# Kernel optimization log

Measured on AMD Instinct MI355X. Metric: run time of the kernel, lower is better.

The kernel has to match this reference:

```python
import jax, jax.numpy as jnp
import numpy as np

N = 25000
E = 400000
HIDDEN = 512
NH = 8
DH = HIDDEN // NH


def setup_inputs() -> dict:
    key = jax.random.key(0)
    ks = jax.random.split(key, 10)
    s = 1.0 / np.sqrt(HIDDEN)
    return {
        "h": jax.random.normal(ks[0], (N, HIDDEN), dtype=jnp.float32),
        "Wq": jax.random.normal(ks[1], (HIDDEN, HIDDEN), dtype=jnp.float32) * s,
        "bq": jnp.zeros((HIDDEN,), dtype=jnp.float32),
        "Wk": jax.random.normal(ks[2], (HIDDEN, HIDDEN), dtype=jnp.float32) * s,
        "bk": jnp.zeros((HIDDEN,), dtype=jnp.float32),
        "Wo": jax.random.normal(ks[3], (HIDDEN, HIDDEN), dtype=jnp.float32) * s,
        "bo": jnp.zeros((HIDDEN,), dtype=jnp.float32),
        "rows": jax.random.randint(ks[4], (E,), 0, N, dtype=jnp.int32),
        "cols": jax.random.randint(ks[5], (E,), 0, N, dtype=jnp.int32),
    }


def reference(h, Wq, bq, Wk, bk, Wo, bo, rows, cols):
    # Projections; reshape (N, dh, nh) exactly as the source does.
    q = (h @ Wq + bq).reshape(N, DH, NH)
    k = (h @ Wk + bk).reshape(N, DH, NH)
    v = k  # source bug kept faithfully: v = linear_k(h)

    # SDDMM: per-edge, per-head dot product (no 1/sqrt(dh) scaling in source).
    scores = jnp.einsum("edh,edh->eh", q[rows], k[cols])  # [E, NH]

    # Row-wise (source-node) segment softmax per head.
    m = jax.ops.segment_max(scores, rows, num_segments=N)       # [N, NH]
    ex = jnp.exp(scores - m[rows])                              # [E, NH]
    denom = jax.ops.segment_sum(ex, rows, num_segments=N)      # [N, NH]
    attn = ex / denom[rows]                                     # [E, NH]

    # SpMM: out[i] = sum_{j in nbr(i)} attn[ij] * v[j]
    msgs = attn[:, None, :] * v[cols]                           # [E, DH, NH]
    out = jax.ops.segment_sum(msgs, rows, num_segments=N)      # [N, DH, NH]

    return out.reshape(N, HIDDEN) @ Wo + bo
```

## Files before the change

kernel.cpp:

```cpp
#include <hip/hip_runtime.h>
#include <math.h>

typedef unsigned short u16;
typedef unsigned int u32;
typedef __attribute__((ext_vector_type(8))) _Float16 half8;
typedef __attribute__((ext_vector_type(8))) u16 ushort8;
typedef __attribute__((ext_vector_type(4))) float f32x4;

__device__ __forceinline__ float h2f(u16 u) {
    union { u16 u; _Float16 h; } c; c.u = u; return (float)c.h;
}
__device__ __forceinline__ u16 f2h(float f) {
    union { u16 u; _Float16 h; } c; c.h = (_Float16)f; return c.u;
}

__device__ __forceinline__ void gload16(void* lds, const void* g) {
    __builtin_amdgcn_global_load_lds(
        (const __attribute__((address_space(1))) u32*)g,
        (__attribute__((address_space(3))) u32*)lds,
        16, 0, 0);
}

template <int OUTMODE>
__global__ __launch_bounds__(256) void gemm_f16(
    const u16* __restrict__ A, const u16* __restrict__ Bt,
    const float* __restrict__ bias, void* __restrict__ Cout, int Mout)
{
    __shared__ __align__(16) u16 As0[4096], As1[4096], Bs0[4096], Bs1[4096];

    const int tid  = threadIdx.x;
    const int wave = tid >> 6;
    const int lane = tid & 63;
    const int m0 = blockIdx.x * 128;
    const int n0 = blockIdx.y * 128;
    const int wr = (wave >> 1) * 64;
    const int wc = (wave & 1) * 64;

    f32x4 acc[4][4];
#pragma unroll
    for (int i = 0; i < 4; ++i)
#pragma unroll
        for (int j = 0; j < 4; ++j) acc[i][j] = (f32x4){0.f, 0.f, 0.f, 0.f};

    const int srow  = lane >> 2;
    const int scolG = ((lane & 3) ^ ((srow >> 1) & 3)) * 8;
    const size_t gOffA = (size_t)(m0 + wave * 32 + srow) * 512 + scolG;
    const size_t gOffB = (size_t)(n0 + wave * 32 + srow) * 512 + scolG;
    const int lOff = wave * 1024 + srow * 32 + (lane & 3) * 8;

    const int fR = ((lane & 15) >> 1) & 3;
    const int paOff = (wr + (lane & 15)) * 32 + ((lane >> 4) ^ fR) * 8;
    const int pbOff = (wc + (lane & 15)) * 32 + ((lane >> 4) ^ fR) * 8;

    auto STAGE = [&](u16* sa, u16* sb, int ko) {
        gload16(sa + lOff,       A  + gOffA + ko);
        gload16(sa + lOff + 512, A  + gOffA + ko + 16 * 512);
        gload16(sb + lOff,       Bt + gOffB + ko);
        gload16(sb + lOff + 512, Bt + gOffB + ko + 16 * 512);
    };
    auto COMPUTE = [&](const u16* sa, const u16* sb) {
        half8 af[4], bf[4];
#pragma unroll
        for (int i = 0; i < 4; ++i) af[i] = *(const half8*)(sa + paOff + i * 512);
#pragma unroll
        for (int j = 0; j < 4; ++j) bf[j] = *(const half8*)(sb + pbOff + j * 512);
#pragma unroll
        for (int i = 0; i < 4; ++i)
#pragma unroll
            for (int j = 0; j < 4; ++j)
                acc[i][j] = __builtin_amdgcn_mfma_f32_16x16x32_f16(
                    af[i], bf[j], acc[i][j], 0, 0, 0);
    };

    STAGE(As0, Bs0, 0);
    __syncthreads();
#pragma unroll
    for (int kt = 0; kt < 16; kt += 2) {
        STAGE(As1, Bs1, (kt + 1) * 32);
        COMPUTE(As0, Bs0);
        __syncthreads();
        if (kt + 2 < 16) STAGE(As0, Bs0, (kt + 2) * 32);
        COMPUTE(As1, Bs1);
        __syncthreads();
    }

    const int ccol  = n0 + wc + (lane & 15);
    const int crow0 = m0 + wr + (lane >> 4) * 4;
#pragma unroll
    for (int j = 0; j < 4; ++j) {
        const float b = bias[ccol + j * 16];
#pragma unroll
        for (int i = 0; i < 4; ++i) {
#pragma unroll
            for (int r = 0; r < 4; ++r) {
                int row = crow0 + i * 16 + r;
                if (row < Mout) {
                    float v = acc[i][j][r] + b;
                    size_t off = (size_t)row * 512 + ccol + j * 16;
                    if (OUTMODE == 0) ((float*)Cout)[off] = v;
                    else              ((u16*)Cout)[off] = f2h(v);
                }
            }
        }
    }
}

__global__ __launch_bounds__(256) void conv_h(
    const float* __restrict__ h, u16* __restrict__ hh, int nN)
{
    int t = blockIdx.x * 256 + threadIdx.x;
    size_t e = (size_t)t * 8;
    int row = (int)(e >> 9);
    ushort8 o;
    if (row < nN) {
        f32x4 a = *(const f32x4*)(h + e);
        f32x4 b = *(const f32x4*)(h + e + 4);
        float x[8] = {a.x, a.y, a.z, a.w, b.x, b.y, b.z, b.w};
#pragma unroll
        for (int i = 0; i < 8; ++i) o[i] = f2h(x[i]);
    } else {
        o = (ushort8){0,0,0,0,0,0,0,0};
    }
    *(ushort8*)(hh + e) = o;
}

__global__ __launch_bounds__(256) void conv_w(
    const float* __restrict__ Wq, const float* __restrict__ Wk,
    const float* __restrict__ Wo, const float* __restrict__ bq,
    const float* __restrict__ bk,
    u16* __restrict__ Wqt, u16* __restrict__ Wkt, u16* __restrict__ Wot,
    float* __restrict__ bqp, float* __restrict__ bkp)
{
    __shared__ float T[64][65];
    const int tid = threadIdx.x;
    const int z = blockIdx.z;
    const int X = blockIdx.x * 64;
    const int Y = blockIdx.y * 64;

    const int r4 = tid >> 4;
    const int c4 = (tid & 15) * 4;
    if (z < 2) {
        const float* W = z ? Wk : Wq;
#pragma unroll
        for (int rr = 0; rr < 64; rr += 16) {
            f32x4 v = *(const f32x4*)(W + (size_t)(X + rr + r4) * 512 + Y + c4);
            T[rr + r4][c4 + 0] = v.x; T[rr + r4][c4 + 1] = v.y;
            T[rr + r4][c4 + 2] = v.z; T[rr + r4][c4 + 3] = v.w;
        }
    } else {
#pragma unroll
        for (int rr = 0; rr < 64; rr += 16) {
            int p2 = (rr + r4) * 8 + (X >> 6);
            f32x4 v = *(const f32x4*)(Wo + (size_t)p2 * 512 + Y + c4);
            T[rr + r4][c4 + 0] = v.x; T[rr + r4][c4 + 1] = v.y;
            T[rr + r4][c4 + 2] = v.z; T[rr + r4][c4 + 3] = v.w;
        }
    }
    __syncthreads();

    const int cc = tid >> 2;
    const int ks = (tid & 3) * 16;
    const int pc = Y + cc;
    const int ro = (z < 2) ? ((pc & 7) * 64 + (pc >> 3)) : pc;
    ushort8 h0, h1;
#pragma unroll
    for (int t = 0; t < 8; ++t) {
        h0[t] = f2h(T[ks + t][cc]);
        h1[t] = f2h(T[ks + 8 + t][cc]);
    }
    size_t o = (size_t)ro * 512 + X + ks;
    if (z == 0) {
        *(ushort8*)(Wqt + o) = h0; *(ushort8*)(Wqt + o + 8) = h1;
    } else if (z == 1) {
        *(ushort8*)(Wkt + o) = h0; *(ushort8*)(Wkt + o + 8) = h1;
    } else {
        *(ushort8*)(Wot + o) = h0; *(ushort8*)(Wot + o + 8) = h1;
        if (blockIdx.x == 0 && blockIdx.y == 0) {
            for (int b = tid; b < 512; b += 256) {
                int pp = (b & 63) * 8 + (b >> 6);
                bqp[b] = bq[pp];
                bkp[b] = bk[pp];
            }
        }
    }
}

__global__ void hist_kernel(const int* __restrict__ rows, int* __restrict__ deg, int E)
{
    int i = blockIdx.x * 256 + threadIdx.x;
    if (i < E) atomicAdd(&deg[rows[i]], 1);
}

#define SCAN_CHUNK 2048

__global__ __launch_bounds__(256) void scan_partial(
    const int* __restrict__ deg, int* __restrict__ bsum, int n)
{
    int base = blockIdx.x * SCAN_CHUNK;
    int t = threadIdx.x;
    int s = 0;
    for (int i = t; i < SCAN_CHUNK; i += 256) {
        int g = base + i;
        s += (g < n) ? deg[g] : 0;
    }
#pragma unroll
    for (int off = 1; off < 64; off <<= 1) s += __shfl_xor(s, off, 64);
    __shared__ int ws[4];
    if ((t & 63) == 0) ws[t >> 6] = s;
    __syncthreads();
    if (t == 0) bsum[blockIdx.x] = ws[0] + ws[1] + ws[2] + ws[3];
}

__global__ __launch_bounds__(64) void scan_bsum(
    int* __restrict__ bsum, int nb, int* __restrict__ rowptr, int n)
{
    int l = threadIdx.x;
    int v = (l < nb) ? bsum[l] : 0;
    int orig = v;
#pragma unroll
    for (int off = 1; off < 64; off <<= 1) {
        int x = __shfl_up(v, off, 64);
        if (l >= off) v += x;
    }
    if (l < nb) bsum[l] = v - orig;
    if (l == nb - 1) rowptr[n] = v;
}

__global__ __launch_bounds__(256) void scan_final(
    const int* __restrict__ deg, const int* __restrict__ bsum,
    int* __restrict__ rowptr, int* __restrict__ cursor, int n)
{
    int t = threadIdx.x;
    int base = blockIdx.x * SCAN_CHUNK + t * 8;
    int v[8];
    int s = 0;
#pragma unroll
    for (int i = 0; i < 8; ++i) {
        int g = base + i;
        v[i] = (g < n) ? deg[g] : 0;
        s += v[i];
    }
    int lane = t & 63, w = t >> 6;
    int inc = s;
#pragma unroll
    for (int off = 1; off < 64; off <<= 1) {
        int x = __shfl_up(inc, off, 64);
        if (lane >= off) inc += x;
    }
    __shared__ int wsum[4];
    if (lane == 63) wsum[w] = inc;
    __syncthreads();
    int excl = bsum[blockIdx.x] + inc - s;
    for (int i = 0; i < w; ++i) excl += wsum[i];
#pragma unroll
    for (int i = 0; i < 8; ++i) {
        int g = base + i;
        if (g < n) { rowptr[g] = excl; cursor[g] = excl; }
        excl += v[i];
    }
}

__global__ void scatter_kernel(const int* __restrict__ rows, const int* __restrict__ cols,
                               int* __restrict__ cursor, int* __restrict__ colc, int E)
{
    int i = blockIdx.x * 256 + threadIdx.x;
    if (i < E) {
        int pos = atomicAdd(&cursor[rows[i]], 1);
        colc[pos] = cols[i];
    }
}

__global__ __launch_bounds__(256) void node_agg(
    const u16* __restrict__ Qh, const u16* __restrict__ Kb,
    const int* __restrict__ rowptr, const int* __restrict__ colc,
    u16* __restrict__ aggb, int nN)
{
    int node = blockIdx.x * 4 + (threadIdx.x >> 6);
    int lane = threadIdx.x & 63;
    if (node >= nN) return;
    size_t base = (size_t)node * 512 + lane * 8;

    float q[8];
    {
        ushort8 qv = __builtin_nontemporal_load((const ushort8*)(Qh + base));
#pragma unroll
        for (int i = 0; i < 8; ++i) q[i] = h2f(qv[i]);
    }

    int start = rowptr[node];
    int deg   = rowptr[node + 1] - start;
    const int* cp = colc + start;
    const size_t loff = (size_t)lane * 8;

    float m = -__builtin_inff();
    float den = 0.f;
    float acc[8];
#pragma unroll
    for (int i = 0; i < 8; ++i) acc[i] = 0.f;

    if (deg > 0) {
        const int dl = deg - 1;
        ushort8 k0 = *(const ushort8*)(Kb + (size_t)cp[0] * 512 + loff);
        ushort8 k1 = *(const ushort8*)(Kb + (size_t)cp[1 < dl ? 1 : dl] * 512 + loff);
        ushort8 k2 = *(const ushort8*)(Kb + (size_t)cp[2 < dl ? 2 : dl] * 512 + loff);
        ushort8 k3 = *(const ushort8*)(Kb + (size_t)cp[3 < dl ? 3 : dl] * 512 + loff);
        for (int j = 0; j < deg; j += 4) {
            int i4 = j + 4 < dl ? j + 4 : dl;
            int i5 = j + 5 < dl ? j + 5 : dl;
            int i6 = j + 6 < dl ? j + 6 : dl;
            int i7 = j + 7 < dl ? j + 7 : dl;
            ushort8 n0 = *(const ushort8*)(Kb + (size_t)cp[i4] * 512 + loff);
            ushort8 n1 = *(const ushort8*)(Kb + (size_t)cp[i5] * 512 + loff);
            ushort8 n2 = *(const ushort8*)(Kb + (size_t)cp[i6] * 512 + loff);
            ushort8 n3 = *(const ushort8*)(Kb + (size_t)cp[i7] * 512 + loff);

            float kf0[8], kf1[8], kf2[8], kf3[8];
#pragma unroll
            for (int i = 0; i < 8; ++i) {
                kf0[i] = h2f(k0[i]); kf1[i] = h2f(k1[i]);
                kf2[i] = h2f(k2[i]); kf3[i] = h2f(k3[i]);
            }
            float p0 = 0.f, p1 = 0.f, p2 = 0.f, p3 = 0.f;
#pragma unroll
            for (int i = 0; i < 8; ++i) {
                p0 = fmaf(q[i], kf0[i], p0);
                p1 = fmaf(q[i], kf1[i], p1);
                p2 = fmaf(q[i], kf2[i], p2);
                p3 = fmaf(q[i], kf3[i], p3);
            }
#pragma unroll
            for (int off = 1; off < 8; off <<= 1) {
                p0 += __shfl_xor(p0, off, 64);
                p1 += __shfl_xor(p1, off, 64);
                p2 += __shfl_xor(p2, off, 64);
                p3 += __shfl_xor(p3, off, 64);
            }

            float pm = fmaxf(fmaxf(p0, p1), fmaxf(p2, p3));
            if (__any(pm > m + 8.f)) {
                float mn = fmaxf(m, pm);
                float sc = __expf(m - mn);
                den *= sc;
#pragma unroll
                for (int i = 0; i < 8; ++i) acc[i] *= sc;
                m = mn;
            }
            float w0 = __expf(p0 - m);
            float w1 = (j + 1 < deg) ? __expf(p1 - m) : 0.f;
            float w2 = (j + 2 < deg) ? __expf(p2 - m) : 0.f;
            float w3 = (j + 3 < deg) ? __expf(p3 - m) : 0.f;
            den += (w0 + w1) + (w2 + w3);
#pragma unroll
            for (int i = 0; i < 8; ++i)
                acc[i] = fmaf(w3, kf3[i], fmaf(w2, kf2[i],
                         fmaf(w1, kf1[i], fmaf(w0, kf0[i], acc[i]))));
            k0 = n0; k1 = n1; k2 = n2; k3 = n3;
        }
    }

    float inv = (deg > 0) ? 1.f / den : 0.f;
    ushort8 o;
#pragma unroll
    for (int i = 0; i < 8; ++i) o[i] = f2h(acc[i] * inv);
    __builtin_nontemporal_store(o, (ushort8*)(aggb + base));
}

extern "C" void kernel_launch(void* const* d_in, const int* in_sizes, int n_in,
                              void* d_out, int out_size, void* d_ws, size_t ws_size,
                              hipStream_t stream)
{
    const float* h  = (const float*)d_in[0];
    const float* Wq = (const float*)d_in[1];
    const float* bq = (const float*)d_in[2];
    const float* Wk = (const float*)d_in[3];
    const float* bk = (const float*)d_in[4];
    const float* Wo = (const float*)d_in[5];
    const float* bo = (const float*)d_in[6];
    const int* rows = (const int*)d_in[7];
    const int* cols = (const int*)d_in[8];
    float* out = (float*)d_out;

    const int HID = 512;
    const int nN  = in_sizes[0] / HID;
    const int E   = in_sizes[7];
    const int nPad = (nN + 127) & ~127;
    const int nb = (nN + SCAN_CHUNK - 1) / SCAN_CHUNK;

    char* w = (char*)d_ws;
    u16* Kb  = (u16*)w;  w += (size_t)nPad * HID * 2;
    u16* hh  = (u16*)w;  w += (size_t)nPad * HID * 2;
    u16* Qh  = (u16*)w;  w += (size_t)nPad * HID * 2;
    u16* Wqt = (u16*)w;  w += 512 * 512 * 2;
    u16* Wkt = (u16*)w;  w += 512 * 512 * 2;
    u16* Wot = (u16*)w;  w += 512 * 512 * 2;
    float* bqp = (float*)w;  w += 512 * 4;
    float* bkp = (float*)w;  w += 512 * 4;
    int* rowptr = (int*)w;   w += (size_t)(nN + 1) * 4;
    int* cursor = (int*)w;   w += (size_t)nN * 4;
    int* deg    = (int*)w;   w += (size_t)nN * 4;
    int* bsum   = (int*)w;   w += 64 * 4;
    int* colc   = (int*)w;

    hipMemsetAsync(deg, 0, (size_t)nN * sizeof(int), stream);
    hist_kernel<<<(E + 255) / 256, 256, 0, stream>>>(rows, deg, E);
    scan_partial<<<nb, 256, 0, stream>>>(deg, bsum, nN);
    scan_bsum<<<1, 64, 0, stream>>>(bsum, nb, rowptr, nN);
    scan_final<<<nb, 256, 0, stream>>>(deg, bsum, rowptr, cursor, nN);
    scatter_kernel<<<(E + 255) / 256, 256, 0, stream>>>(rows, cols, cursor, colc, E);

    conv_h<<<(nPad * (HID / 8) + 255) / 256, 256, 0, stream>>>(h, hh, nN);
    conv_w<<<dim3(8, 8, 3), 256, 0, stream>>>(Wq, Wk, Wo, bq, bk,
                                              Wqt, Wkt, Wot, bqp, bkp);

    dim3 gg(nPad / 128, 4);
    gemm_f16<1><<<gg, 256, 0, stream>>>(hh, Wqt, bqp, Qh, nPad);
    gemm_f16<1><<<gg, 256, 0, stream>>>(hh, Wkt, bkp, Kb, nPad);

    node_agg<<<(nN + 3) / 4, 256, 0, stream>>>(Qh, Kb, rowptr, colc, hh, nN);

    gemm_f16<0><<<gg, 256, 0, stream>>>(hh, Wot, bo, out, nN);
}
```

Before: 263.7 us.

## Fuse prep kernels, merge Q/K GEMMs, and use packed fp16 math in aggregation

Merges the h conversion, degree histogram and weight transpose into one prep launch. It folds the bsum scan into scan_final and runs the Q and K projections as one GEMM launch via blockIdx.z. The node aggregation now uses fdot2 for the dot products and packed fp16 accumulation for the weighted sum, with a tighter rescale threshold. The aim is fewer launches and less conversion ALU work. Accumulating in fp16 risks precision loss and overflow on high-degree nodes.

New measurement: 234.8 us. 1.12x faster.

```diff
diff --git a/kernel.cpp b/kernel.cpp
--- a/kernel.cpp
+++ b/kernel.cpp
@@ -4,15 +4,20 @@
 typedef unsigned short u16;
 typedef unsigned int u32;
 typedef __attribute__((ext_vector_type(8))) _Float16 half8;
+typedef __attribute__((ext_vector_type(2))) _Float16 half2v;
 typedef __attribute__((ext_vector_type(8))) u16 ushort8;
 typedef __attribute__((ext_vector_type(4))) float f32x4;
 
-__device__ __forceinline__ float h2f(u16 u) {
-    union { u16 u; _Float16 h; } c; c.u = u; return (float)c.h;
-}
 __device__ __forceinline__ u16 f2h(float f) {
     union { u16 u; _Float16 h; } c; c.h = (_Float16)f; return c.u;
 }
+
+#if __has_builtin(__builtin_amdgcn_fdot2)
+#define FDOT2(a, b, c) __builtin_amdgcn_fdot2((a), (b), (c), false)
+#else
+#define FDOT2(a, b, c) fmaf((float)(a)[0], (float)(b)[0], \
+                        fmaf((float)(a)[1], (float)(b)[1], (c)))
+#endif
 
 __device__ __forceinline__ void gload16(void* lds, const void* g) {
     __builtin_amdgcn_global_load_lds(
@@ -22,17 +27,13 @@
 }
 
 template <int OUTMODE>
-__global__ __launch_bounds__(256) void gemm_f16(
-    const u16* __restrict__ A, const u16* __restrict__ Bt,
-    const float* __restrict__ bias, void* __restrict__ Cout, int Mout)
-{
-    __shared__ __align__(16) u16 As0[4096], As1[4096], Bs0[4096], Bs1[4096];
-
+__device__ __forceinline__ void gemm_body(
+    const u16* A, const u16* Bt, const float* bias, void* Cout, int Mout,
+    int m0, int n0, u16* As0, u16* As1, u16* Bs0, u16* Bs1)
+{
     const int tid  = threadIdx.x;
     const int wave = tid >> 6;
     const int lane = tid & 63;
-    const int m0 = blockIdx.x * 128;
-    const int n0 = blockIdx.y * 128;
     const int wr = (wave >> 1) * 64;
     const int wc = (wave & 1) * 64;
 
@@ -105,37 +106,69 @@
     }
 }
 
-__global__ __launch_bounds__(256) void conv_h(
-    const float* __restrict__ h, u16* __restrict__ hh, int nN)
-{
-    int t = blockIdx.x * 256 + threadIdx.x;
-    size_t e = (size_t)t * 8;
-    int row = (int)(e >> 9);
-    ushort8 o;
-    if (row < nN) {
-        f32x4 a = *(const f32x4*)(h + e);
-        f32x4 b = *(const f32x4*)(h + e + 4);
-        float x[8] = {a.x, a.y, a.z, a.w, b.x, b.y, b.z, b.w};
-#pragma unroll
-        for (int i = 0; i < 8; ++i) o[i] = f2h(x[i]);
-    } else {
-        o = (ushort8){0,0,0,0,0,0,0,0};
-    }
-    *(ushort8*)(hh + e) = o;
-}
-
-__global__ __launch_bounds__(256) void conv_w(
+__global__ __launch_bounds__(256) void gemm_qk(
+    const u16* __restrict__ hh, const u16* __restrict__ Wqt,
+    const u16* __restrict__ Wkt, const float* __restrict__ bqp,
+    const float* __restrict__ bkp, u16* __restrict__ Qh,
+    u16* __restrict__ Kb, int nPad)
+{
+    __shared__ __align__(16) u16 As0[4096], As1[4096], Bs0[4096], Bs1[4096];
+    const u16* Bt = blockIdx.z ? Wkt : Wqt;
+    const float* bias = blockIdx.z ? bkp : bqp;
+    u16* out = blockIdx.z ? Kb : Qh;
+    gemm_body<1>(hh, Bt, bias, out, nPad, blockIdx.x * 128, blockIdx.y * 128,
+                 As0, As1, Bs0, Bs1);
+}
+
+__global__ __launch_bounds__(256) void gemm_wo(
+    const u16* __restrict__ A, const u16* __restrict__ Wot,
+    const float* __restrict__ bo, float* __restrict__ C, int Mout)
+{
+    __shared__ __align__(16) u16 As0[4096], As1[4096], Bs0[4096], Bs1[4096];
+    gemm_body<0>(A, Wot, bo, C, Mout, blockIdx.x * 128, blockIdx.y * 128,
+                 As0, As1, Bs0, Bs1);
+}
+
+__global__ __launch_bounds__(256) void prep(
+    const float* __restrict__ h, u16* __restrict__ hh, int nN,
+    const int* __restrict__ rows, int* __restrict__ deg, int E,
     const float* __restrict__ Wq, const float* __restrict__ Wk,
     const float* __restrict__ Wo, const float* __restrict__ bq,
     const float* __restrict__ bk,
     u16* __restrict__ Wqt, u16* __restrict__ Wkt, u16* __restrict__ Wot,
-    float* __restrict__ bqp, float* __restrict__ bkp)
+    float* __restrict__ bqp, float* __restrict__ bkp,
+    int nbH, int nbE)
 {
     __shared__ float T[64][65];
     const int tid = threadIdx.x;
-    const int z = blockIdx.z;
-    const int X = blockIdx.x * 64;
-    const int Y = blockIdx.y * 64;
+    const int b = blockIdx.x;
+
+    if (b < nbH) {
+        int t = b * 256 + tid;
+        size_t e = (size_t)t * 8;
+        int row = (int)(e >> 9);
+        ushort8 o;
+        if (row < nN) {
+            f32x4 a = *(const f32x4*)(h + e);
+            f32x4 bb = *(const f32x4*)(h + e + 4);
+            float x[8] = {a.x, a.y, a.z, a.w, bb.x, bb.y, bb.z, bb.w};
+#pragma unroll
+            for (int i = 0; i < 8; ++i) o[i] = f2h(x[i]);
+        } else {
+            o = (ushort8){0,0,0,0,0,0,0,0};
+        }
+        *(ushort8*)(hh + e) = o;
+        return;
+    }
+    if (b < nbH + nbE) {
+        int i = (b - nbH) * 256 + tid;
+        if (i < E) atomicAdd(&deg[rows[i]], 1);
+        return;
+    }
+    int rem = b - nbH - nbE;
+    const int z = rem >> 6;
+    const int X = (rem & 7) * 64;
+    const int Y = ((rem >> 3) & 7) * 64;
 
     const int r4 = tid >> 4;
     const int c4 = (tid & 15) * 4;
@@ -175,20 +208,14 @@
         *(ushort8*)(Wkt + o) = h0; *(ushort8*)(Wkt + o + 8) = h1;
     } else {
         *(ushort8*)(Wot + o) = h0; *(ushort8*)(Wot + o + 8) = h1;
-        if (blockIdx.x == 0 && blockIdx.y == 0) {
-            for (int b = tid; b < 512; b += 256) {
-                int pp = (b & 63) * 8 + (b >> 6);
-                bqp[b] = bq[pp];
-                bkp[b] = bk[pp];
-            }
-        }
-    }
-}
-
-__global__ void hist_kernel(const int* __restrict__ rows, int* __restrict__ deg, int E)
-{
-    int i = blockIdx.x * 256 + threadIdx.x;
-    if (i < E) atomicAdd(&deg[rows[i]], 1);
+        if (rem == 128) {
+            for (int bi = tid; bi < 512; bi += 256) {
+                int pp = (bi & 63) * 8 + (bi >> 6);
+                bqp[bi] = bq[pp];
+                bkp[bi] = bk[pp];
+            }
+        }
+    }
 }
 
 #define SCAN_CHUNK 2048
@@ -211,25 +238,16 @@
     if (t == 0) bsum[blockIdx.x] = ws[0] + ws[1] + ws[2] + ws[3];
 }
 
-__global__ __launch_bounds__(64) void scan_bsum(
-    int* __restrict__ bsum, int nb, int* __restrict__ rowptr, int n)
-{
-    int l = threadIdx.x;
-    int v = (l < nb) ? bsum[l] : 0;
-    int orig = v;
-#pragma unroll
-    for (int off = 1; off < 64; off <<= 1) {
-        int x = __shfl_up(v, off, 64);
-        if (l >= off) v += x;
-    }
-    if (l < nb) bsum[l] = v - orig;
-    if (l == nb - 1) rowptr[n] = v;
-}
-
 __global__ __launch_bounds__(256) void scan_final(
     const int* __restrict__ deg, const int* __restrict__ bsum,
-    int* __restrict__ rowptr, int* __restrict__ cursor, int n)
-{
+    int* __restrict__ rowptr, int* __restrict__ cursor, int n, int nb)
+{
+    int boff = 0, total = 0;
+    for (int i = 0; i < nb; ++i) {
+        int v = bsum[i];
+        if (i < (int)blockIdx.x) boff += v;
+        total += v;
+    }
     int t = threadIdx.x;
     int base = blockIdx.x * SCAN_CHUNK + t * 8;
     int v[8];
@@ -250,7 +268,7 @@
     __shared__ int wsum[4];
     if (lane == 63) wsum[w] = inc;
     __syncthreads();
-    int excl = bsum[blockIdx.x] + inc - s;
+    int excl = boff + inc - s;
     for (int i = 0; i < w; ++i) excl += wsum[i];
 #pragma unroll
     for (int i = 0; i < 8; ++i) {
@@ -258,6 +276,7 @@
         if (g < n) { rowptr[g] = excl; cursor[g] = excl; }
         excl += v[i];
     }
+    if (blockIdx.x == 0 && t == 0) rowptr[n] = total;
 }
 
 __global__ void scatter_kernel(const int* __restrict__ rows, const int* __restrict__ cols,
@@ -280,12 +299,10 @@
     if (node >= nN) return;
     size_t base = (size_t)node * 512 + lane * 8;
 
-    float q[8];
-    {
-        ushort8 qv = __builtin_nontemporal_load((const ushort8*)(Qh + base));
-#pragma unroll
-        for (int i = 0; i < 8; ++i) q[i] = h2f(qv[i]);
-    }
+    half8 qv = __builtin_nontemporal_load((const half8*)(Qh + base));
+    half2v q2[4];
+#pragma unroll
+    for (int i = 0; i < 4; ++i) q2[i] = (half2v){qv[2 * i], qv[2 * i + 1]};
 
     int start = rowptr[node];
     int deg   = rowptr[node + 1] - start;
@@ -294,39 +311,38 @@
 
     float m = -__builtin_inff();
     float den = 0.f;
-    float acc[8];
-#pragma unroll
-    for (int i = 0; i < 8; ++i) acc[i] = 0.f;
+    half2v acc2[4];
+#pragma unroll
+    for (int i = 0; i < 4; ++i) acc2[i] = (half2v){(_Float16)0.f, (_Float16)0.f};
 
     if (deg > 0) {
         const int dl = deg - 1;
-        ushort8 k0 = *(const ushort8*)(Kb + (size_t)cp[0] * 512 + loff);
-        ushort8 k1 = *(const ushort8*)(Kb + (size_t)cp[1 < dl ? 1 : dl] * 512 + loff);
-        ushort8 k2 = *(const ushort8*)(Kb + (size_t)cp[2 < dl ? 2 : dl] * 512 + loff);
-        ushort8 k3 = *(const ushort8*)(Kb + (size_t)cp[3 < dl ? 3 : dl] * 512 + loff);
+        half8 k0 = *(const half8*)(Kb + (size_t)cp[0] * 512 + loff);
+        half8 k1 = *(const half8*)(Kb + (size_t)cp[1 < dl ? 1 : dl] * 512 + loff);
+        half8 k2 = *(const half8*)(Kb + (size_t)cp[2 < dl ? 2 : dl] * 512 + loff);
+        half8 k3 = *(const half8*)(Kb + (size_t)cp[3 < dl ? 3 : dl] * 512 + loff);
         for (int j = 0; j < deg; j += 4) {
             int i4 = j + 4 < dl ? j + 4 : dl;
             int i5 = j + 5 < dl ? j + 5 : dl;
             int i6 = j + 6 < dl ? j + 6 : dl;
             int i7 = j + 7 < dl ? j + 7 : dl;
-            ushort8 n0 = *(const ushort8*)(Kb + (size_t)cp[i4] * 512 + loff);
-            ushort8 n1 = *(const ushort8*)(Kb + (size_t)cp[i5] * 512 + loff);
-            ushort8 n2 = *(const ushort8*)(Kb + (size_t)cp[i6] * 512 + loff);
-            ushort8 n3 = *(const ushort8*)(Kb + (size_t)cp[i7] * 512 + loff);
-
-            float kf0[8], kf1[8], kf2[8], kf3[8];
-#pragma unroll
-            for (int i = 0; i < 8; ++i) {
-                kf0[i] = h2f(k0[i]); kf1[i] = h2f(k1[i]);
-                kf2[i] = h2f(k2[i]); kf3[i] = h2f(k3[i]);
-            }
+            half8 n0 = *(const half8*)(Kb + (size_t)cp[i4] * 512 + loff);
+            half8 n1 = *(const half8*)(Kb + (size_t)cp[i5] * 512 + loff);
+            half8 n2 = *(const half8*)(Kb + (size_t)cp[i6] * 512 + loff);
+            half8 n3 = *(const half8*)(Kb + (size_t)cp[i7] * 512 + loff);
+
             float p0 = 0.f, p1 = 0.f, p2 = 0.f, p3 = 0.f;
 #pragma unroll
-            for (int i = 0; i < 8; ++i) {
-                p0 = fmaf(q[i], kf0[i], p0);
-                p1 = fmaf(q[i], kf1[i], p1);
-                p2 = fmaf(q[i], kf2[i], p2);
-                p3 = fmaf(q[i], kf3[i], p3);
+            for (int i = 0; i < 4; ++i) {
+                half2v a = q2[i];
+                half2v b0 = (half2v){k0[2 * i], k0[2 * i + 1]};
+                half2v b1 = (half2v){k1[2 * i], k1[2 * i + 1]};
+                half2v b2 = (half2v){k2[2 * i], k2[2 * i + 1]};
+                half2v b3 = (half2v){k3[2 * i], k3[2 * i + 1]};
+                p0 = FDOT2(a, b0, p0);
+                p1 = FDOT2(a, b1, p1);
+                p2 = FDOT2(a, b2, p2);
+                p3 = FDOT2(a, b3, p3);
             }
 #pragma unroll
             for (int off = 1; off < 8; off <<= 1) {
@@ -337,12 +353,14 @@
             }
 
             float pm = fmaxf(fmaxf(p0, p1), fmaxf(p2, p3));
-            if (__any(pm > m + 8.f)) {
+            if (__any(pm > m + 4.f)) {
                 float mn = fmaxf(m, pm);
                 float sc = __expf(m - mn);
                 den *= sc;
-#pragma unroll
-                for (int i = 0; i < 8; ++i) acc[i] *= sc;
+                _Float16 sch = (_Float16)sc;
+                half2v sc2 = {sch, sch};
+#pragma unroll
+                for (int i = 0; i < 4; ++i) acc2[i] *= sc2;
                 m = mn;
             }
             float w0 = __expf(p0 - m);
@@ -350,10 +368,20 @@
             float w2 = (j + 2 < deg) ? __expf(p2 - m) : 0.f;
             float w3 = (j + 3 < deg) ? __expf(p3 - m) : 0.f;
             den += (w0 + w1) + (w2 + w3);
-#pragma unroll
-            for (int i = 0; i < 8; ++i)
-                acc[i] = fmaf(w3, kf3[i], fmaf(w2, kf2[i],
-                         fmaf(w1, kf1[i], fmaf(w0, kf0[i], acc[i]))));
+            _Float16 h0 = (_Float16)w0, h1 = (_Float16)w1;
+            _Float16 h2 = (_Float16)w2, h3 = (_Float16)w3;
+            half2v w02 = {h0, h0}, w12 = {h1, h1}, w22 = {h2, h2}, w32 = {h3, h3};
+#pragma unroll
+            for (int i = 0; i < 4; ++i) {
+                half2v b0 = (half2v){k0[2 * i], k0[2 * i + 1]};
+                half2v b1 = (half2v){k1[2 * i], k1[2 * i + 1]};
+                half2v b2 = (half2v){k2[2 * i], k2[2 * i + 1]};
+                half2v b3 = (half2v){k3[2 * i], k3[2 * i + 1]};
+                acc2[i] += w02 * b0;
+                acc2[i] += w12 * b1;
+                acc2[i] += w22 * b2;
+                acc2[i] += w32 * b3;
+            }
             k0 = n0; k1 = n1; k2 = n2; k3 = n3;
         }
     }
@@ -361,7 +389,10 @@
     float inv = (deg > 0) ? 1.f / den : 0.f;
     ushort8 o;
 #pragma unroll
-    for (int i = 0; i < 8; ++i) o[i] = f2h(acc[i] * inv);
+    for (int i = 0; i < 4; ++i) {
+        o[2 * i]     = f2h((float)acc2[i][0] * inv);
+        o[2 * i + 1] = f2h((float)acc2[i][1] * inv);
+    }
     __builtin_nontemporal_store(o, (ushort8*)(aggb + base));
 }
 
@@ -385,6 +416,8 @@
     const int E   = in_sizes[7];
     const int nPad = (nN + 127) & ~127;
     const int nb = (nN + SCAN_CHUNK - 1) / SCAN_CHUNK;
+    const int nbH = nPad * (HID / 8) / 256;
+    const int nbE = (E + 255) / 256;
 
     char* w = (char*)d_ws;
     u16* Kb  = (u16*)w;  w += (size_t)nPad * HID * 2;
@@ -401,22 +434,20 @@
     int* bsum   = (int*)w;   w += 64 * 4;
     int* colc   = (int*)w;
 
-    hipMemsetAsync(deg, 0, (size_t)nN * sizeof(int), stream);
-    hist_kernel<<<(E + 255) / 256, 256, 0, stream>>>(rows, deg, E);
+    (void)hipMemsetAsync(deg, 0, (size_t)nN * sizeof(int), stream);
+
+    prep<<<nbH + nbE + 192, 256, 0, stream>>>(
+        h, hh, nN, rows, deg, E, Wq, Wk, Wo, bq, bk,
+        Wqt, Wkt, Wot, bqp, bkp, nbH, nbE);
+
     scan_partial<<<nb, 256, 0, stream>>>(deg, bsum, nN);
-    scan_bsum<<<1, 64, 0, stream>>>(bsum, nb, rowptr, nN);
-    scan_final<<<nb, 256, 0, stream>>>(deg, bsum, rowptr, cursor, nN);
+    scan_final<<<nb, 256, 0, stream>>>(deg, bsum, rowptr, cursor, nN, nb);
     scatter_kernel<<<(E + 255) / 256, 256, 0, stream>>>(rows, cols, cursor, colc, E);
 
-    conv_h<<<(nPad * (HID / 8) + 255) / 256, 256, 0, stream>>>(h, hh, nN);
-    conv_w<<<dim3(8, 8, 3), 256, 0, stream>>>(Wq, Wk, Wo, bq, bk,
-                                              Wqt, Wkt, Wot, bqp, bkp);
-
-    dim3 gg(nPad / 128, 4);
-    gemm_f16<1><<<gg, 256, 0, stream>>>(hh, Wqt, bqp, Qh, nPad);
-    gemm_f16<1><<<gg, 256, 0, stream>>>(hh, Wkt, bkp, Kb, nPad);
+    gemm_qk<<<dim3(nPad / 128, 4, 2), 256, 0, stream>>>(
+        hh, Wqt, Wkt, bqp, bkp, Qh, Kb, nPad);
 
     node_agg<<<(nN + 3) / 4, 256, 0, stream>>>(Qh, Kb, rowptr, colc, hh, nN);
 
-    gemm_f16<0><<<gg, 256, 0, stream>>>(hh, Wot, bo, out, nN);
-}
+    gemm_wo<<<dim3(nPad / 128, 4), 256, 0, stream>>>(hh, Wot, bo, out, nN);
+}
```
